# Performance work log

Hardware: AMD Instinct MI355X
Metric: run time of the kernel (lower is better)

Reference implementation:

```python
import jax, jax.numpy as jnp
import numpy as np


def setup_inputs() -> dict:
    key = jax.random.key(0)
    k1, k2 = jax.random.split(key)
    B, P, d, C = 8, 4096, 256, 1024
    x = jax.random.normal(k1, (B, P, d), dtype=jnp.float32)
    # encoder weight initialized with std=0.001 as in nn.init.normal_(..., std=0.001)
    W = jax.random.normal(k2, (C, d), dtype=jnp.float32) * 0.001
    return {"x": x, "W": W}


def reference(x, W):
    # x: [B, P, d], W: [C, d] (bias of nn.Linear is unused in forward)
    B, P, d = x.shape
    C = W.shape[0]
    # scores = relu(x @ W^T): [B, P, C]
    scores = jax.nn.relu(jnp.einsum('bpd,cd->bpc', x, W))
    # per-channel argmax over patch dim P (torch argmax after transpose(1,2))
    idx = jnp.argmax(scores, axis=1)  # [B, C], values in [0, P)
    # scatter_add: output[b, idx[b,c], :] += W[c, :]
    out = jnp.zeros((B, P, d), dtype=x.dtype)
    out = out.at[jnp.arange(B)[:, None], idx].add(
        jnp.broadcast_to(W, (B, C, d)))
    return out
```

## Files before the change

kernel.cpp:

```cpp
#include <hip/hip_runtime.h>
#include <cstdint>

#define BB 8
#define PP 4096
#define DD 256
#define CC 1024

#define XT_BYTES (33554432ull)
#define WT_BYTES (1048576ull)
#define TILE_BYTES 131072ull

typedef _Float16 f16x8 __attribute__((ext_vector_type(8)));
typedef float f32x16 __attribute__((ext_vector_type(16)));
typedef unsigned long long u64;

__device__ __forceinline__ void async_load16(const void* src, void* lds_dst) {
    __builtin_amdgcn_global_load_lds(
        (const __attribute__((address_space(1))) uint32_t*)src,
        (__attribute__((address_space(3))) uint32_t*)lds_dst,
        16, 0, 0);
}

__global__ __launch_bounds__(256) void init_ws_kernel(u64* keys, int n) {
    int i = blockIdx.x * 256 + threadIdx.x;
    if (i < n) keys[i] = 0x00000000FFFFFFFFull;
}

__global__ __launch_bounds__(256) void transform_kernel(
    const float* __restrict__ x, const float* __restrict__ W,
    char* __restrict__ xT, char* __restrict__ wT, u64* __restrict__ keys)
{
    __shared__ float ls[64 * 260];

    const int id = blockIdx.x;
    const int t = threadIdx.x;
    if (id < 32) keys[id * 256 + t] = 0x00000000FFFFFFFFull;

    const int tile = id >> 1;
    const int h = id & 1;
    const float* src;
    char* dstTile;
    if (tile < 256) {
        src = x + (size_t)tile * 128 * 256;
        dstTile = xT + (size_t)tile * TILE_BYTES;
    } else {
        int cy = tile - 256;
        src = W + (size_t)cy * 128 * 256;
        dstTile = wT + (size_t)cy * TILE_BYTES;
    }

    #pragma unroll
    for (int i = 0; i < 16; ++i) {
        int c = i * 256 + t;
        int row = c >> 6, kq = c & 63;
        float4 v = *reinterpret_cast<const float4*>(
            src + ((size_t)(h * 64 + row)) * 256 + kq * 4);
        *reinterpret_cast<float4*>(&ls[row * 260 + kq * 4]) = v;
    }
    __syncthreads();

    #pragma unroll
    for (int j = 0; j < 16; ++j) {
        int q = j * 256 + t;
        int slot = q & 63;
        int sp = (q >> 6) & 1;
        int rtl = (q >> 7) & 1;
        int k16 = q >> 8;
        int rowl = rtl * 32 + (slot & 31);
        int k = k16 * 16 + (slot >> 5) * 8;
        const float* p = &ls[rowl * 260 + k];
        f16x8 o;
        if (sp == 0) {
            #pragma unroll
            for (int i = 0; i < 8; ++i) o[i] = (_Float16)p[i];
        } else {
            #pragma unroll
            for (int i = 0; i < 8; ++i) {
                _Float16 hv = (_Float16)p[i];
                o[i] = (_Float16)((p[i] - (float)hv) * 4096.0f);
            }
        }
        int rt = h * 2 + rtl;
        size_t off = (((size_t)k16 * 4 + rt) * 2 + sp) * 1024 + (size_t)slot * 16;
        *reinterpret_cast<f16x8*>(dstTile + off) = o;
    }
}

__global__ __launch_bounds__(512, 2) void gemm_argmax_p_kernel(
    const char* __restrict__ xT, const char* __restrict__ wT,
    u64* __restrict__ keys)
{
    __shared__ __align__(16) char lds[3][24576];
    __shared__ u64 smax[128];

    const int tid = threadIdx.x;
    const int lane = tid & 63;
    const int wid = tid >> 6;
    const int wm = wid >> 1;
    const int wn = wid & 1;
    const int q  = blockIdx.x;
    const int cy = blockIdx.y;
    const int b  = blockIdx.z;
    const int p0 = q * 256;
    const int c0 = cy * 128;

    const char* aTile0 = xT + ((size_t)(b * 32 + q * 2)) * TILE_BYTES;
    const char* bChunk = wT + (size_t)cy * TILE_BYTES;

    const char* sSrc[3];
    int sDst[3];
    #pragma unroll
    for (int i = 0; i < 3; ++i) {
        int c = wid * 3 + i;
        if (c < 16) {
            int half = c >> 3, rt4 = (c >> 1) & 3, sp = c & 1;
            sSrc[i] = aTile0 + (size_t)half * TILE_BYTES
                      + (size_t)((rt4 * 2 + sp) << 10) + (size_t)lane * 16;
            sDst[i] = c << 10;
        } else {
            int d = c - 16;
            sSrc[i] = bChunk + (size_t)(d << 10) + (size_t)lane * 16;
            sDst[i] = 16384 + (d << 10);
        }
    }

    f32x16 zero;
    #pragma unroll
    for (int i = 0; i < 16; ++i) zero[i] = 0.f;
    f32x16 acc_hi[2][2], acc_lo[2][2];
    #pragma unroll
    for (int i = 0; i < 2; ++i)
        #pragma unroll
        for (int j = 0; j < 2; ++j) { acc_hi[i][j] = zero; acc_lo[i][j] = zero; }

    const int aOff0 = (((wm * 2 + 0) >> 2) << 13) + ((((wm * 2 + 0) & 3) * 2) << 10) + lane * 16;
    const int aOff1 = (((wm * 2 + 1) >> 2) << 13) + ((((wm * 2 + 1) & 3) * 2) << 10) + lane * 16;
    const int bOff0 = 16384 + (((wn * 2 + 0) * 2) << 10) + lane * 16;
    const int bOff1 = 16384 + (((wn * 2 + 1) * 2) << 10) + lane * 16;

    #pragma unroll
    for (int i = 0; i < 3; ++i) async_load16(sSrc[i], &lds[0][sDst[i]]);
    #pragma unroll
    for (int i = 0; i < 3; ++i) async_load16(sSrc[i] + 8192, &lds[1][sDst[i]]);

    #pragma unroll
    for (int st = 0; st < 16; ++st) {
        const int buf = st % 3;
        if (st < 15) asm volatile("s_waitcnt vmcnt(3)" ::: "memory");
        else         asm volatile("s_waitcnt vmcnt(0)" ::: "memory");
        __builtin_amdgcn_s_barrier();

        const char* L = &lds[buf][0];
        f16x8 a[2][2], bv[2][2];
        a[0][0] = *reinterpret_cast<const f16x8*>(L + aOff0);
        a[0][1] = *reinterpret_cast<const f16x8*>(L + aOff0 + 1024);
        a[1][0] = *reinterpret_cast<const f16x8*>(L + aOff1);
        a[1][1] = *reinterpret_cast<const f16x8*>(L + aOff1 + 1024);
        bv[0][0] = *reinterpret_cast<const f16x8*>(L + bOff0);
        bv[0][1] = *reinterpret_cast<const f16x8*>(L + bOff0 + 1024);
        bv[1][0] = *reinterpret_cast<const f16x8*>(L + bOff1);
        bv[1][1] = *reinterpret_cast<const f16x8*>(L + bOff1 + 1024);

        if (st + 2 < 16) {
            const int nb = (st + 2) % 3;
            #pragma unroll
            for (int i = 0; i < 3; ++i)
                async_load16(sSrc[i] + (size_t)(st + 2) * 8192, &lds[nb][sDst[i]]);
        }

        asm volatile("s_waitcnt lgkmcnt(0)" ::: "memory");
        __builtin_amdgcn_s_setprio(1);
        #pragma unroll
        for (int rt = 0; rt < 2; ++rt)
            #pragma unroll
            for (int ct = 0; ct < 2; ++ct) {
                acc_hi[rt][ct] = __builtin_amdgcn_mfma_f32_32x32x16_f16(
                    a[rt][0], bv[ct][0], acc_hi[rt][ct], 0, 0, 0);
                acc_lo[rt][ct] = __builtin_amdgcn_mfma_f32_32x32x16_f16(
                    a[rt][0], bv[ct][1], acc_lo[rt][ct], 0, 0, 0);
                acc_lo[rt][ct] = __builtin_amdgcn_mfma_f32_32x32x16_f16(
                    a[rt][1], bv[ct][0], acc_lo[rt][ct], 0, 0, 0);
            }
        __builtin_amdgcn_s_setprio(0);
    }

    if (tid < 128) smax[tid] = 0ull;
    __syncthreads();

    #pragma unroll
    for (int ct = 0; ct < 2; ++ct) {
        u64 bk = 0ull;
        #pragma unroll
        for (int rt = 0; rt < 2; ++rt) {
            f32x16 h = acc_hi[rt][ct];
            f32x16 l = acc_lo[rt][ct];
            #pragma unroll
            for (int reg = 0; reg < 16; ++reg) {
                float v = fmaxf(h[reg] + l[reg] * (1.0f / 4096.0f), 0.f);
                int prow = p0 + (wm * 2 + rt) * 32 +
                           (reg & 3) + 8 * (reg >> 2) + 4 * (lane >> 5);
                u64 key = ((u64)__float_as_uint(v) << 32) |
                          (unsigned int)(0xFFFFFFFFu - (unsigned int)prow);
                bk = bk > key ? bk : key;
            }
        }
        u64 other = __shfl_xor(bk, 32, 64);
        bk = bk > other ? bk : other;
        if (lane < 32) {
            int col = (wn * 2 + ct) * 32 + (lane & 31);
            atomicMax(&smax[col], bk);
        }
    }
    __syncthreads();
    if (tid < 128) {
        atomicMax(&keys[(size_t)b * CC + c0 + tid], smax[tid]);
    }
}

__global__ __launch_bounds__(256, 2) void gemm_argmax_conv_kernel(
    const float* __restrict__ x, const float* __restrict__ W,
    u64* __restrict__ keys)
{
    __shared__ f16x8 lA[4][4][2][64];
    __shared__ f16x8 lB[4][4][2][64];

    const int tid = threadIdx.x;
    const int lane = tid & 63;
    const int w = tid >> 6;
    const int wy = w >> 1, wx = w & 1;
    const int p0 = blockIdx.x * 128;
    const int c0 = blockIdx.y * 128;
    const int b  = blockIdx.z;

    const float* xb = x + (size_t)b * PP * DD;

    f32x16 zero;
    #pragma unroll
    for (int i = 0; i < 16; ++i) zero[i] = 0.f;
    f32x16 acc_hi[2][2], acc_lo[2][2];
    #pragma unroll
    for (int i = 0; i < 2; ++i)
        #pragma unroll
        for (int j = 0; j < 2; ++j) { acc_hi[i][j] = zero; acc_lo[i][j] = zero; }

    for (int st = 0; st < 4; ++st) {
        const int k0 = st * 64;
        float4 gA[8], gB[8];
        #pragma unroll
        for (int v = 0; v < 4; ++v) {
            int pi = tid + 256 * v;
            int r  = pi >> 3;
            int ck = (pi & 7) * 8;
            const float* pa = xb + (size_t)(p0 + r) * DD + k0 + ck;
            gA[2 * v]     = *reinterpret_cast<const float4*>(pa);
            gA[2 * v + 1] = *reinterpret_cast<const float4*>(pa + 4);
            const float* pb = W + (size_t)(c0 + r) * DD + k0 + ck;
            gB[2 * v]     = *reinterpret_cast<const float4*>(pb);
            gB[2 * v + 1] = *reinterpret_cast<const float4*>(pb + 4);
        }
        __syncthreads();
        #pragma unroll
        for (int v = 0; v < 4; ++v) {
            int pi = tid + 256 * v;
            int r  = pi >> 3;
            int ph = pi & 7;
            int kk = ph >> 1;
            int half = ph & 1;
            int slot = (r & 31) + 32 * half;
            int rtp = r >> 5;
            float va[8] = {gA[2*v].x, gA[2*v].y, gA[2*v].z, gA[2*v].w,
                           gA[2*v+1].x, gA[2*v+1].y, gA[2*v+1].z, gA[2*v+1].w};
            f16x8 h1, h2;
            #pragma unroll
            for (int i = 0; i < 8; ++i) {
                _Float16 h = (_Float16)va[i];
                h1[i] = h;
                h2[i] = (_Float16)((va[i] - (float)h) * 4096.0f);
            }
            lA[kk][rtp][0][slot] = h1;
            lA[kk][rtp][1][slot] = h2;
            float vb[8] = {gB[2*v].x, gB[2*v].y, gB[2*v].z, gB[2*v].w,
                           gB[2*v+1].x, gB[2*v+1].y, gB[2*v+1].z, gB[2*v+1].w};
            f16x8 g1, g2;
            #pragma unroll
            for (int i = 0; i < 8; ++i) {
                _Float16 h = (_Float16)vb[i];
                g1[i] = h;
                g2[i] = (_Float16)((vb[i] - (float)h) * 4096.0f);
            }
            lB[kk][rtp][0][slot] = g1;
            lB[kk][rtp][1][slot] = g2;
        }
        __syncthreads();
        #pragma unroll
        for (int kk = 0; kk < 4; ++kk) {
            f16x8 xa[2][2], wb2[2][2];
            #pragma unroll
            for (int rt = 0; rt < 2; ++rt) {
                xa[rt][0] = lA[kk][wy * 2 + rt][0][lane];
                xa[rt][1] = lA[kk][wy * 2 + rt][1][lane];
            }
            #pragma unroll
            for (int ct = 0; ct < 2; ++ct) {
                wb2[ct][0] = lB[kk][wx * 2 + ct][0][lane];
                wb2[ct][1] = lB[kk][wx * 2 + ct][1][lane];
            }
            #pragma unroll
            for (int rt = 0; rt < 2; ++rt)
                #pragma unroll
                for (int ct = 0; ct < 2; ++ct) {
                    acc_hi[rt][ct] = __builtin_amdgcn_mfma_f32_32x32x16_f16(
                        xa[rt][0], wb2[ct][0], acc_hi[rt][ct], 0, 0, 0);
                    acc_lo[rt][ct] = __builtin_amdgcn_mfma_f32_32x32x16_f16(
                        xa[rt][0], wb2[ct][1], acc_lo[rt][ct], 0, 0, 0);
                    acc_lo[rt][ct] = __builtin_amdgcn_mfma_f32_32x32x16_f16(
                        xa[rt][1], wb2[ct][0], acc_lo[rt][ct], 0, 0, 0);
                }
        }
    }

    u64* smax = reinterpret_cast<u64*>(&lA[0][0][0][0]);
    __syncthreads();
    if (tid < 128) smax[tid] = 0ull;
    __syncthreads();

    #pragma unroll
    for (int ct = 0; ct < 2; ++ct) {
        u64 bk = 0ull;
        #pragma unroll
        for (int rt = 0; rt < 2; ++rt) {
            f32x16 h = acc_hi[rt][ct];
            f32x16 l = acc_lo[rt][ct];
            #pragma unroll
            for (int reg = 0; reg < 16; ++reg) {
                float v = fmaxf(h[reg] + l[reg] * (1.0f / 4096.0f), 0.f);
                int prow = p0 + (wy * 2 + rt) * 32 +
                           (reg & 3) + 8 * (reg >> 2) + 4 * (lane >> 5);
                u64 key = ((u64)__float_as_uint(v) << 32) |
                          (unsigned int)(0xFFFFFFFFu - (unsigned int)prow);
                bk = bk > key ? bk : key;
            }
        }
        u64 other = __shfl_xor(bk, 32, 64);
        bk = bk > other ? bk : other;
        if (lane < 32) {
            int col = (wx * 2 + ct) * 32 + (lane & 31);
            atomicMax(&smax[col], bk);
        }
    }
    __syncthreads();
    if (tid < 128) {
        atomicMax(&keys[(size_t)b * CC + c0 + tid], smax[tid]);
    }
}

__global__ __launch_bounds__(64) void scatter_kernel(
    const u64* __restrict__ keys,
    const float* __restrict__ W,
    float* __restrict__ out)
{
    const int cell = blockIdx.x;
    const int c = cell & (CC - 1);
    const int b = cell >> 10;
    u64 key = keys[cell];
    unsigned int p = (0xFFFFFFFFu - (unsigned int)(key & 0xFFFFFFFFull)) & (PP - 1);

    const float* wrow = W + (size_t)c * DD;
    float* orow = out + ((size_t)b * PP + p) * DD;
    const int t = threadIdx.x;
    #pragma unroll
    for (int u = 0; u < 4; u++) {
        int idx = u * 64 + t;
        atomicAdd(&orow[idx], wrow[idx]);
    }
}

extern "C" void kernel_launch(void* const* d_in, const int* in_sizes, int n_in,
                              void* d_out, int out_size, void* d_ws, size_t ws_size,
                              hipStream_t stream) {
    const float* x = (const float*)d_in[0];
    const float* W = (const float*)d_in[1];
    float* out = (float*)d_out;

    char* wsb = (char*)d_ws;
    u64* keys = (u64*)wsb;
    char* xT = wsb + 65536;
    char* wT = xT + XT_BYTES;
    const size_t need = 65536 + XT_BYTES + WT_BYTES;

    hipMemsetAsync(d_out, 0, (size_t)out_size * sizeof(float), stream);

    if (ws_size >= need) {
        transform_kernel<<<528, 256, 0, stream>>>(x, W, xT, wT, keys);
        dim3 grid(PP / 256, CC / 128, BB);
        gemm_argmax_p_kernel<<<grid, 512, 0, stream>>>(xT, wT, keys);
    } else {
        int n = BB * CC;
        init_ws_kernel<<<(n + 255) / 256, 256, 0, stream>>>(keys, n);
        dim3 grid(PP / 128, CC / 128, BB);
        gemm_argmax_conv_kernel<<<grid, 256, 0, stream>>>(x, W, keys);
    }

    {
        dim3 grid(BB * CC);
        scatter_kernel<<<grid, 64, 0, stream>>>(keys, W, out);
    }
}
```

Measured before the change: 86.47 us.

## Use single-fp16 GEMM pass with margin-based fp32 rescue for ambiguous argmax

Drops the hi/lo split-fp16 emulation of fp32 and computes scores with a single fp16 MFMA pass, tracking the top score and runner-up per channel. A finalize kernel flags channels whose winning margin is below a fixed threshold (or whose top score is tiny), and a rescue kernel recomputes those channels exactly in fp32 from the original x. This cuts MFMA work and the transformed-x traffic by about two thirds. In exchange it adds two kernels, and correctness now rests on the error bound implied by MARGIN; the rescue cost depends on how many channels get flagged.

```diff
diff --git a/kernel.cpp b/kernel.cpp
--- a/kernel.cpp
+++ b/kernel.cpp
@@ -6,9 +6,17 @@
 #define DD 256
 #define CC 1024
 
-#define XT_BYTES (33554432ull)
-#define WT_BYTES (1048576ull)
-#define TILE_BYTES 131072ull
+#define TILE_H 65536ull
+#define MARGIN 2.5e-4f
+
+#define WS_KEYS 0ull
+#define WS_PK   65536ull
+#define WS_PS   1114112ull
+#define WS_CNT  1638400ull
+#define WS_LIST 1638528ull
+#define WS_XT   1671296ull
+#define WS_WT   18448512ull
+#define WS_NEED 18972800ull
 
 typedef _Float16 f16x8 __attribute__((ext_vector_type(8)));
 typedef float f32x16 __attribute__((ext_vector_type(16)));
@@ -21,6 +29,10 @@
         16, 0, 0);
 }
 
+__device__ __forceinline__ float keyscore(u64 k) {
+    return __uint_as_float((unsigned int)(k >> 32));
+}
+
 __global__ __launch_bounds__(256) void init_ws_kernel(u64* keys, int n) {
     int i = blockIdx.x * 256 + threadIdx.x;
     if (i < n) keys[i] = 0x00000000FFFFFFFFull;
@@ -28,25 +40,23 @@
 
 __global__ __launch_bounds__(256) void transform_kernel(
     const float* __restrict__ x, const float* __restrict__ W,
-    char* __restrict__ xT, char* __restrict__ wT, u64* __restrict__ keys)
+    char* __restrict__ xT, char* __restrict__ wT)
 {
     __shared__ float ls[64 * 260];
 
     const int id = blockIdx.x;
     const int t = threadIdx.x;
-    if (id < 32) keys[id * 256 + t] = 0x00000000FFFFFFFFull;
-
     const int tile = id >> 1;
     const int h = id & 1;
     const float* src;
     char* dstTile;
     if (tile < 256) {
         src = x + (size_t)tile * 128 * 256;
-        dstTile = xT + (size_t)tile * TILE_BYTES;
+        dstTile = xT + (size_t)tile * TILE_H;
     } else {
         int cy = tile - 256;
         src = W + (size_t)cy * 128 * 256;
-        dstTile = wT + (size_t)cy * TILE_BYTES;
+        dstTile = wT + (size_t)cy * TILE_H;
     }
 
     #pragma unroll
@@ -60,88 +70,72 @@
     __syncthreads();
 
     #pragma unroll
-    for (int j = 0; j < 16; ++j) {
-        int q = j * 256 + t;
-        int slot = q & 63;
-        int sp = (q >> 6) & 1;
-        int rtl = (q >> 7) & 1;
-        int k16 = q >> 8;
+    for (int j = 0; j < 8; ++j) {
+        int q2 = j * 256 + t;
+        int slot = q2 & 63;
+        int rtl = (q2 >> 6) & 1;
+        int k16 = q2 >> 7;
         int rowl = rtl * 32 + (slot & 31);
         int k = k16 * 16 + (slot >> 5) * 8;
         const float* p = &ls[rowl * 260 + k];
         f16x8 o;
-        if (sp == 0) {
-            #pragma unroll
-            for (int i = 0; i < 8; ++i) o[i] = (_Float16)p[i];
-        } else {
-            #pragma unroll
-            for (int i = 0; i < 8; ++i) {
-                _Float16 hv = (_Float16)p[i];
-                o[i] = (_Float16)((p[i] - (float)hv) * 4096.0f);
-            }
-        }
+        #pragma unroll
+        for (int i = 0; i < 8; ++i) o[i] = (_Float16)p[i];
         int rt = h * 2 + rtl;
-        size_t off = (((size_t)k16 * 4 + rt) * 2 + sp) * 1024 + (size_t)slot * 16;
+        size_t off = ((size_t)(k16 * 4 + rt) << 10) + (size_t)slot * 16;
         *reinterpret_cast<f16x8*>(dstTile + off) = o;
     }
 }
 
-__global__ __launch_bounds__(512, 2) void gemm_argmax_p_kernel(
+__global__ __launch_bounds__(256, 2) void pass1_kernel(
     const char* __restrict__ xT, const char* __restrict__ wT,
-    u64* __restrict__ keys)
+    u64* __restrict__ part_k1, float* __restrict__ part_s2)
 {
-    __shared__ __align__(16) char lds[3][24576];
-    __shared__ u64 smax[128];
+    __shared__ __align__(16) char lds[3][12288];
 
     const int tid = threadIdx.x;
     const int lane = tid & 63;
-    const int wid = tid >> 6;
-    const int wm = wid >> 1;
-    const int wn = wid & 1;
+    const int wm = tid >> 6;
     const int q  = blockIdx.x;
     const int cy = blockIdx.y;
     const int b  = blockIdx.z;
     const int p0 = q * 256;
     const int c0 = cy * 128;
 
-    const char* aTile0 = xT + ((size_t)(b * 32 + q * 2)) * TILE_BYTES;
-    const char* bChunk = wT + (size_t)cy * TILE_BYTES;
+    const char* aTile0 = xT + ((size_t)(b * 32 + q * 2)) * TILE_H;
+    const char* bTile  = wT + (size_t)cy * TILE_H;
 
     const char* sSrc[3];
     int sDst[3];
     #pragma unroll
     for (int i = 0; i < 3; ++i) {
-        int c = wid * 3 + i;
-        if (c < 16) {
-            int half = c >> 3, rt4 = (c >> 1) & 3, sp = c & 1;
-            sSrc[i] = aTile0 + (size_t)half * TILE_BYTES
-                      + (size_t)((rt4 * 2 + sp) << 10) + (size_t)lane * 16;
+        int c = wm * 3 + i;
+        if (c < 8) {
+            sSrc[i] = aTile0 + (size_t)(c >> 2) * TILE_H
+                      + (size_t)((c & 3) << 10) + (size_t)lane * 16;
             sDst[i] = c << 10;
         } else {
-            int d = c - 16;
-            sSrc[i] = bChunk + (size_t)(d << 10) + (size_t)lane * 16;
-            sDst[i] = 16384 + (d << 10);
+            sSrc[i] = bTile + (size_t)((c - 8) << 10) + (size_t)lane * 16;
+            sDst[i] = 8192 + ((c - 8) << 10);
         }
     }
 
     f32x16 zero;
     #pragma unroll
     for (int i = 0; i < 16; ++i) zero[i] = 0.f;
-    f32x16 acc_hi[2][2], acc_lo[2][2];
+    f32x16 acc[2][4];
     #pragma unroll
     for (int i = 0; i < 2; ++i)
         #pragma unroll
-        for (int j = 0; j < 2; ++j) { acc_hi[i][j] = zero; acc_lo[i][j] = zero; }
-
-    const int aOff0 = (((wm * 2 + 0) >> 2) << 13) + ((((wm * 2 + 0) & 3) * 2) << 10) + lane * 16;
-    const int aOff1 = (((wm * 2 + 1) >> 2) << 13) + ((((wm * 2 + 1) & 3) * 2) << 10) + lane * 16;
-    const int bOff0 = 16384 + (((wn * 2 + 0) * 2) << 10) + lane * 16;
-    const int bOff1 = 16384 + (((wn * 2 + 1) * 2) << 10) + lane * 16;
+        for (int j = 0; j < 4; ++j) acc[i][j] = zero;
+
+    const int aOff0 = ((wm * 2 + 0) << 10) + lane * 16;
+    const int aOff1 = ((wm * 2 + 1) << 10) + lane * 16;
 
     #pragma unroll
     for (int i = 0; i < 3; ++i) async_load16(sSrc[i], &lds[0][sDst[i]]);
     #pragma unroll
-    for (int i = 0; i < 3; ++i) async_load16(sSrc[i] + 8192, &lds[1][sDst[i]]);
+    for (int i = 0; i < 3; ++i) async_load16(sSrc[i] + 4096, &lds[1][sDst[i]]);
 
     #pragma unroll
     for (int st = 0; st < 16; ++st) {
@@ -151,21 +145,18 @@
         __builtin_amdgcn_s_barrier();
 
         const char* L = &lds[buf][0];
-        f16x8 a[2][2], bv[2][2];
-        a[0][0] = *reinterpret_cast<const f16x8*>(L + aOff0);
-        a[0][1] = *reinterpret_cast<const f16x8*>(L + aOff0 + 1024);
-        a[1][0] = *reinterpret_cast<const f16x8*>(L + aOff1);
-        a[1][1] = *reinterpret_cast<const f16x8*>(L + aOff1 + 1024);
-        bv[0][0] = *reinterpret_cast<const f16x8*>(L + bOff0);
-        bv[0][1] = *reinterpret_cast<const f16x8*>(L + bOff0 + 1024);
-        bv[1][0] = *reinterpret_cast<const f16x8*>(L + bOff1);
-        bv[1][1] = *reinterpret_cast<const f16x8*>(L + bOff1 + 1024);
+        f16x8 a[2], bv[4];
+        a[0] = *reinterpret_cast<const f16x8*>(L + aOff0);
+        a[1] = *reinterpret_cast<const f16x8*>(L + aOff1);
+        #pragma unroll
+        for (int ct = 0; ct < 4; ++ct)
+            bv[ct] = *reinterpret_cast<const f16x8*>(L + 8192 + (ct << 10) + lane * 16);
 
         if (st + 2 < 16) {
             const int nb = (st + 2) % 3;
             #pragma unroll
             for (int i = 0; i < 3; ++i)
-                async_load16(sSrc[i] + (size_t)(st + 2) * 8192, &lds[nb][sDst[i]]);
+                async_load16(sSrc[i] + (size_t)(st + 2) * 4096, &lds[nb][sDst[i]]);
         }
 
         asm volatile("s_waitcnt lgkmcnt(0)" ::: "memory");
@@ -173,47 +164,162 @@
         #pragma unroll
         for (int rt = 0; rt < 2; ++rt)
             #pragma unroll
-            for (int ct = 0; ct < 2; ++ct) {
-                acc_hi[rt][ct] = __builtin_amdgcn_mfma_f32_32x32x16_f16(
-                    a[rt][0], bv[ct][0], acc_hi[rt][ct], 0, 0, 0);
-                acc_lo[rt][ct] = __builtin_amdgcn_mfma_f32_32x32x16_f16(
-                    a[rt][0], bv[ct][1], acc_lo[rt][ct], 0, 0, 0);
-                acc_lo[rt][ct] = __builtin_amdgcn_mfma_f32_32x32x16_f16(
-                    a[rt][1], bv[ct][0], acc_lo[rt][ct], 0, 0, 0);
-            }
+            for (int ct = 0; ct < 4; ++ct)
+                acc[rt][ct] = __builtin_amdgcn_mfma_f32_32x32x16_f16(
+                    a[rt], bv[ct], acc[rt][ct], 0, 0, 0);
         __builtin_amdgcn_s_setprio(0);
     }
 
-    if (tid < 128) smax[tid] = 0ull;
-    __syncthreads();
-
-    #pragma unroll
-    for (int ct = 0; ct < 2; ++ct) {
-        u64 bk = 0ull;
+    __syncthreads();
+    u64*  pk = reinterpret_cast<u64*>(&lds[0][0]);
+    float* ps = reinterpret_cast<float*>(&lds[0][4096]);
+
+    #pragma unroll
+    for (int ct = 0; ct < 4; ++ct) {
+        u64 k1 = 0ull;
+        float s2 = 0.f;
         #pragma unroll
         for (int rt = 0; rt < 2; ++rt) {
-            f32x16 h = acc_hi[rt][ct];
-            f32x16 l = acc_lo[rt][ct];
+            f32x16 v16 = acc[rt][ct];
             #pragma unroll
             for (int reg = 0; reg < 16; ++reg) {
-                float v = fmaxf(h[reg] + l[reg] * (1.0f / 4096.0f), 0.f);
-                int prow = p0 + (wm * 2 + rt) * 32 +
+                float v = fmaxf(v16[reg], 0.f);
+                int prow = p0 + wm * 64 + rt * 32 +
                            (reg & 3) + 8 * (reg >> 2) + 4 * (lane >> 5);
                 u64 key = ((u64)__float_as_uint(v) << 32) |
                           (unsigned int)(0xFFFFFFFFu - (unsigned int)prow);
-                bk = bk > key ? bk : key;
-            }
-        }
-        u64 other = __shfl_xor(bk, 32, 64);
-        bk = bk > other ? bk : other;
+                if (key > k1) { s2 = fmaxf(s2, keyscore(k1)); k1 = key; }
+                else          { s2 = fmaxf(s2, v); }
+            }
+        }
+        u64 ok = __shfl_xor(k1, 32, 64);
+        float os2 = __shfl_xor(s2, 32, 64);
+        if (ok > k1) { s2 = fmaxf(fmaxf(s2, os2), keyscore(k1)); k1 = ok; }
+        else         { s2 = fmaxf(fmaxf(s2, os2), keyscore(ok)); }
         if (lane < 32) {
-            int col = (wn * 2 + ct) * 32 + (lane & 31);
-            atomicMax(&smax[col], bk);
+            int col = ct * 32 + lane;
+            pk[wm * 128 + col] = k1;
+            ps[wm * 128 + col] = s2;
         }
     }
     __syncthreads();
     if (tid < 128) {
-        atomicMax(&keys[(size_t)b * CC + c0 + tid], smax[tid]);
+        int col = tid;
+        u64 K = pk[col];
+        float S = ps[col];
+        #pragma unroll
+        for (int w2 = 1; w2 < 4; ++w2) {
+            u64 k2 = pk[w2 * 128 + col];
+            float s2b = ps[w2 * 128 + col];
+            if (k2 > K) { S = fmaxf(fmaxf(S, s2b), keyscore(K)); K = k2; }
+            else        { S = fmaxf(fmaxf(S, s2b), keyscore(k2)); }
+        }
+        int cell = b * CC + c0 + col;
+        part_k1[(size_t)cell * 16 + q] = K;
+        part_s2[(size_t)cell * 16 + q] = S;
+    }
+}
+
+__global__ __launch_bounds__(256) void finalize_kernel(
+    const u64* __restrict__ part_k1, const float* __restrict__ part_s2,
+    u64* __restrict__ keys, int* __restrict__ cnt, int* __restrict__ blist)
+{
+    int cell = blockIdx.x * 256 + threadIdx.x;
+    u64 K = part_k1[(size_t)cell * 16];
+    float S = part_s2[(size_t)cell * 16];
+    #pragma unroll
+    for (int q = 1; q < 16; ++q) {
+        u64 k2 = part_k1[(size_t)cell * 16 + q];
+        float s2b = part_s2[(size_t)cell * 16 + q];
+        if (k2 > K) { S = fmaxf(fmaxf(S, s2b), keyscore(K)); K = k2; }
+        else        { S = fmaxf(fmaxf(S, s2b), keyscore(k2)); }
+    }
+    float s1 = keyscore(K);
+    bool flag = (s1 - S < MARGIN) || (s1 < MARGIN);
+    if (!flag) {
+        keys[cell] = K;
+    } else {
+        keys[cell] = 0ull;
+        int b = cell >> 10;
+        int i = atomicAdd(&cnt[b], 1);
+        blist[b * 1024 + i] = cell & (CC - 1);
+    }
+}
+
+__global__ __launch_bounds__(256, 2) void rescue_kernel(
+    const float* __restrict__ x, const float* __restrict__ W,
+    const int* __restrict__ cnt, const int* __restrict__ blist,
+    u64* __restrict__ keys)
+{
+    __shared__ float xs[64][265];
+    __shared__ float rsum[64][5];
+
+    const int rc = blockIdx.x;
+    const int b  = blockIdx.y;
+    const int n = cnt[b];
+    if (n == 0) return;
+    const int tid = threadIdx.x;
+
+    const float* xb = x + ((size_t)b * PP + (size_t)rc * 64) * DD;
+    #pragma unroll
+    for (int i = 0; i < 16; ++i) {
+        int idx = i * 256 + tid;
+        int r = idx >> 6, c4 = (idx & 63) * 4;
+        float4 v = *reinterpret_cast<const float4*>(xb + (size_t)r * DD + c4);
+        xs[r][c4 + 0] = v.x; xs[r][c4 + 1] = v.y;
+        xs[r][c4 + 2] = v.z; xs[r][c4 + 3] = v.w;
+    }
+    __syncthreads();
+
+    const int r = tid & 63;
+    const int kq = tid >> 6;
+    for (int j = 0; j < n; ++j) {
+        int c = blist[b * 1024 + j];
+        const float* wr = W + (size_t)c * DD + kq * 64;
+        const float* xr = &xs[r][kq * 64];
+        float a0 = 0.f, a1 = 0.f;
+        #pragma unroll
+        for (int i = 0; i < 64; i += 2) {
+            a0 = fmaf(xr[i], wr[i], a0);
+            a1 = fmaf(xr[i + 1], wr[i + 1], a1);
+        }
+        rsum[r][kq] = a0 + a1;
+        __syncthreads();
+        if (tid < 64) {
+            float s = (rsum[tid][0] + rsum[tid][1]) + (rsum[tid][2] + rsum[tid][3]);
+            float v = fmaxf(s, 0.f);
+            int p = rc * 64 + tid;
+            u64 key = ((u64)__float_as_uint(v) << 32) |
+                      (unsigned int)(0xFFFFFFFFu - (unsigned int)p);
+            #pragma unroll
+            for (int off = 1; off < 64; off <<= 1) {
+                u64 o = __shfl_xor(key, off, 64);
+                key = key > o ? key : o;
+            }
+            if (tid == 0) atomicMax(&keys[b * CC + c], key);
+        }
+        __syncthreads();
+    }
+}
+
+__global__ __launch_bounds__(64) void scatter_kernel(
+    const u64* __restrict__ keys,
+    const float* __restrict__ W,
+    float* __restrict__ out)
+{
+    const int cell = blockIdx.x;
+    const int c = cell & (CC - 1);
+    const int b = cell >> 10;
+    u64 key = keys[cell];
+    unsigned int p = (0xFFFFFFFFu - (unsigned int)(key & 0xFFFFFFFFull)) & (PP - 1);
+
+    const float* wrow = W + (size_t)c * DD;
+    float* orow = out + ((size_t)b * PP + p) * DD;
+    const int t = threadIdx.x;
+    #pragma unroll
+    for (int u = 0; u < 4; u++) {
+        int idx = u * 64 + t;
+        atomicAdd(&orow[idx], wrow[idx]);
     }
 }
 
@@ -354,27 +460,6 @@
     }
 }
 
-__global__ __launch_bounds__(64) void scatter_kernel(
-    const u64* __restrict__ keys,
-    const float* __restrict__ W,
-    float* __restrict__ out)
-{
-    const int cell = blockIdx.x;
-    const int c = cell & (CC - 1);
-    const int b = cell >> 10;
-    u64 key = keys[cell];
-    unsigned int p = (0xFFFFFFFFu - (unsigned int)(key & 0xFFFFFFFFull)) & (PP - 1);
-
-    const float* wrow = W + (size_t)c * DD;
-    float* orow = out + ((size_t)b * PP + p) * DD;
-    const int t = threadIdx.x;
-    #pragma unroll
-    for (int u = 0; u < 4; u++) {
-        int idx = u * 64 + t;
-        atomicAdd(&orow[idx], wrow[idx]);
-    }
-}
-
 extern "C" void kernel_launch(void* const* d_in, const int* in_sizes, int n_in,
                               void* d_out, int out_size, void* d_ws, size_t ws_size,
                               hipStream_t stream) {
@@ -383,17 +468,28 @@
     float* out = (float*)d_out;
 
     char* wsb = (char*)d_ws;
-    u64* keys = (u64*)wsb;
-    char* xT = wsb + 65536;
-    char* wT = xT + XT_BYTES;
-    const size_t need = 65536 + XT_BYTES + WT_BYTES;
+    u64* keys    = (u64*)(wsb + WS_KEYS);
+    u64* part_k1 = (u64*)(wsb + WS_PK);
+    float* part_s2 = (float*)(wsb + WS_PS);
+    int* cnt     = (int*)(wsb + WS_CNT);
+    int* blist   = (int*)(wsb + WS_LIST);
+    char* xT     = wsb + WS_XT;
+    char* wT     = wsb + WS_WT;
 
     hipMemsetAsync(d_out, 0, (size_t)out_size * sizeof(float), stream);
 
-    if (ws_size >= need) {
-        transform_kernel<<<528, 256, 0, stream>>>(x, W, xT, wT, keys);
-        dim3 grid(PP / 256, CC / 128, BB);
-        gemm_argmax_p_kernel<<<grid, 512, 0, stream>>>(xT, wT, keys);
+    if (ws_size >= WS_NEED) {
+        hipMemsetAsync(cnt, 0, 32, stream);
+        transform_kernel<<<528, 256, 0, stream>>>(x, W, xT, wT);
+        {
+            dim3 grid(PP / 256, CC / 128, BB);
+            pass1_kernel<<<grid, 256, 0, stream>>>(xT, wT, part_k1, part_s2);
+        }
+        finalize_kernel<<<32, 256, 0, stream>>>(part_k1, part_s2, keys, cnt, blist);
+        {
+            dim3 grid(64, BB);
+            rescue_kernel<<<grid, 256, 0, stream>>>(x, W, cnt, blist, keys);
+        }
     } else {
         int n = BB * CC;
         init_ws_kernel<<<(n + 255) / 256, 256, 0, stream>>>(keys, n);
```

Result: slower. 152.2 us (+76.0%).
